# Kernel tuning notes

Measured on AMD Instinct MI355X. Metric: run time of the kernel, lower is better.

The kernel has to match this reference:

```python
import jax, jax.numpy as jnp
import numpy as np


def setup_inputs() -> dict:
    key = jax.random.key(0)
    k_h, k_w1, k_w2 = jax.random.split(key, 3)
    B, S, D = 8, 2048, 1024
    H = 2 * D  # reasoning_net hidden width
    # xavier_uniform-style scaled weights
    lim1 = float(np.sqrt(6.0 / (D + H)))
    lim2 = float(np.sqrt(6.0 / (H + D)))
    return {
        "hidden_states": jax.random.normal(k_h, (B, S, D), dtype=jnp.float32),
        "W1": jax.random.uniform(k_w1, (D, H), dtype=jnp.float32, minval=-lim1, maxval=lim1),
        "b1": jnp.zeros((H,), dtype=jnp.float32),
        "W2": jax.random.uniform(k_w2, (H, D), dtype=jnp.float32, minval=-lim2, maxval=lim2),
        "b2": jnp.zeros((D,), dtype=jnp.float32),
    }


def reference(hidden_states, W1, b1, W2, b2):
    """Chain reasoning forward.

    The torch loop carries output[:, -1:], but reasoning_net is a per-token MLP
    (Linear over the last dim), so processed[:, -1:] == MLP(current token) and the
    carried state never influences appended outputs. Faithful closed form:
      out[:, 0]  = hidden_states[:, 0]
      out[:, i]  = MLP(hidden_states[:, i])  for i >= 1
    Dropout is identity (eval). GELU is exact (torch default).
    """
    rest = hidden_states[:, 1:, :]  # [B, S-1, D]
    h = jax.nn.gelu(jnp.einsum("bsd,dh->bsh", rest, W1) + b1, approximate=False)
    out_rest = jnp.einsum("bsh,hd->bsd", h, W2) + b2
    return jnp.concatenate([hidden_states[:, :1, :], out_rest], axis=1)
```

## Files before the change

kernel.cpp:

```cpp
#include <hip/hip_runtime.h>
#include <hip/hip_bf16.h>
#include <cstdint>
#include <cstddef>

typedef unsigned short u16;
typedef __attribute__((ext_vector_type(8))) __bf16 bf16x8;
typedef __attribute__((ext_vector_type(8))) unsigned short u16x8;
typedef __attribute__((ext_vector_type(4))) float f32x4;

__device__ __forceinline__ void gload_lds16(const void* g, void* l) {
    __builtin_amdgcn_global_load_lds(
        (const __attribute__((address_space(1))) unsigned int*)g,
        (__attribute__((address_space(3))) unsigned int*)l,
        16, 0, 0);
}

__device__ __forceinline__ u16 f2bf(float f) {
    union { float f; unsigned int u; } v; v.f = f;
    unsigned int r = v.u + 0x7fffu + ((v.u >> 16) & 1u);
    return (u16)(r >> 16);
}

__device__ __forceinline__ float gelu_tanh(float x) {
    const float z = 0.7978845608028654f * x * (1.0f + 0.044715f * x * x);
    const float t = __builtin_amdgcn_exp2f(2.885390081777927f * z);
    const float th = 1.0f - 2.0f * __builtin_amdgcn_rcpf(t + 1.0f);
    return 0.5f * x * (1.0f + th);
}

template <int GELU, int OUT_BF16, int SKIP_S>
__global__ void gemm_bt(const u16* __restrict__ A,
                        const u16* __restrict__ Bt,
                        const float* __restrict__ bias,
                        void* __restrict__ Cv,
                        int M, int N, int K, int row0) {
    __shared__ __align__(16) char smem[32768];
    u16* As = (u16*)smem;
    u16* Bs = (u16*)(smem + 16384);
    float* Ct = (float*)smem;

    const int tid  = threadIdx.x;
    const int lane = tid & 63;
    const int wave = tid >> 6;
    const int wm   = (wave >> 1) * 64;
    const int wn   = (wave & 1) * 64;
    const int mrow = lane & 15;
    const int half = lane >> 4;

    const size_t ldb = (size_t)K * 2;
    const char* Ab = (const char*)(A + (size_t)blockIdx.x * 128 * K);
    const char* Bb = (const char*)(Bt + (size_t)blockIdx.y * 128 * K);

    size_t goff[4];
    int loff[4];
#pragma unroll
    for (int i = 0; i < 4; ++i) {
        const int L = tid + 256 * i, r = L >> 3, s = L & 7;
        goff[i] = (size_t)r * ldb + (size_t)((s ^ (r & 7)) << 4);
        loff[i] = L << 4;
    }

    int alds[2][4], blds[2][4];
#pragma unroll
    for (int j = 0; j < 2; ++j)
#pragma unroll
        for (int t = 0; t < 4; ++t) {
            const int g = j * 4 + half;
            const int ra = wm + t * 16 + mrow;
            alds[j][t] = ra * 128 + ((g ^ (ra & 7)) << 4);
            const int rb = wn + t * 16 + mrow;
            blds[j][t] = rb * 128 + ((g ^ (rb & 7)) << 4);
        }

    f32x4 acc[4][4];
#pragma unroll
    for (int i = 0; i < 4; ++i)
#pragma unroll
        for (int j = 0; j < 4; ++j) acc[i][j] = f32x4{0.f, 0.f, 0.f, 0.f};

    for (int k0 = 0; k0 < K; k0 += 64) {
        const size_t kb = (size_t)k0 * 2;
#pragma unroll
        for (int i = 0; i < 4; ++i)
            gload_lds16(Ab + goff[i] + kb, (char*)As + loff[i]);
#pragma unroll
        for (int i = 0; i < 4; ++i)
            gload_lds16(Bb + goff[i] + kb, (char*)Bs + loff[i]);
        __syncthreads();

#pragma unroll
        for (int j = 0; j < 2; ++j) {
            bf16x8 af[4], bfr[4];
#pragma unroll
            for (int t = 0; t < 4; ++t) {
                af[t]  = *(const bf16x8*)((const char*)As + alds[j][t]);
                bfr[t] = *(const bf16x8*)((const char*)Bs + blds[j][t]);
            }
#pragma unroll
            for (int mi = 0; mi < 4; ++mi)
#pragma unroll
                for (int ni = 0; ni < 4; ++ni)
                    acc[mi][ni] = __builtin_amdgcn_mfma_f32_16x16x32_bf16(
                        af[mi], bfr[ni], acc[mi][ni], 0, 0, 0);
        }
        __syncthreads();
    }

    const int lrow0 = wm + half * 4;
    const int lcol0 = wn + mrow;
    const int growbase = blockIdx.x * 128;
    const int gcolbase = blockIdx.y * 128;
    const int rr_rd = tid >> 3, cs_rd = (tid & 7) * 16;

#pragma unroll
    for (int c = 0; c < 4; ++c) {
        __syncthreads();
        if ((wm >> 6) == (c >> 1)) {
            const int mi0 = (c & 1) * 2;
#pragma unroll
            for (int dmi = 0; dmi < 2; ++dmi) {
                const int mi = mi0 + dmi;
#pragma unroll
                for (int ni = 0; ni < 4; ++ni) {
                    const int col = lcol0 + ni * 16;
                    const float bv = bias[gcolbase + col];
#pragma unroll
                    for (int r = 0; r < 4; ++r) {
                        const int rr = (mi * 16 + lrow0 + r) & 31;
                        float v = acc[mi][ni][r] + bv;
                        if (GELU) v = gelu_tanh(v);
                        Ct[rr * 132 + col] = v;
                    }
                }
            }
        }
        __syncthreads();
        const int grow = growbase + 32 * c + rr_rd;
        const bool skip = SKIP_S && (((row0 + grow) & 2047) == 0);
        if (!skip) {
            const float* ct = &Ct[rr_rd * 132 + cs_rd];
            const f32x4 v0 = *(const f32x4*)(ct);
            const f32x4 v1 = *(const f32x4*)(ct + 4);
            const f32x4 v2 = *(const f32x4*)(ct + 8);
            const f32x4 v3 = *(const f32x4*)(ct + 12);
            if (OUT_BF16) {
                u16x8 lo, hi;
#pragma unroll
                for (int j = 0; j < 4; ++j) {
                    lo[j] = f2bf(v0[j]); lo[j + 4] = f2bf(v1[j]);
                    hi[j] = f2bf(v2[j]); hi[j + 4] = f2bf(v3[j]);
                }
                u16* p = (u16*)Cv + (size_t)grow * N + gcolbase + cs_rd;
                *(u16x8*)(p)     = lo;
                *(u16x8*)(p + 8) = hi;
            } else {
                float* p = (float*)Cv + (size_t)grow * N + gcolbase + cs_rd;
                *(f32x4*)(p)      = v0;
                *(f32x4*)(p + 4)  = v1;
                *(f32x4*)(p + 8)  = v2;
                *(f32x4*)(p + 12) = v3;
            }
        }
    }
}

__device__ __forceinline__ void tcvt_block(const float* __restrict__ src,
                                           u16* __restrict__ dst, int R, int C,
                                           int bx, int by, int x, int y,
                                           u16 (*t)[33]) {
    for (int i = 0; i < 32; i += 8)
        t[y + i][x] = f2bf(src[(size_t)(by + y + i) * C + (bx + x)]);
    __syncthreads();
    for (int i = 0; i < 32; i += 8)
        dst[(size_t)(bx + y + i) * R + (by + x)] = t[x][y + i];
}

__global__ void prep(const float* __restrict__ X, const float* __restrict__ W1,
                     const float* __restrict__ W2, u16* __restrict__ Xb,
                     u16* __restrict__ W1T, u16* __restrict__ W2T,
                     float* __restrict__ out, long long nX) {
    __shared__ u16 t[32][33];
    const int b = blockIdx.x, tid = threadIdx.x;
    const int x = tid & 31, y = tid >> 5;
    if (b < 2048) {
        tcvt_block(W1, W1T, 1024, 2048, (b & 63) * 32, (b >> 6) * 32, x, y, t);
    } else if (b < 4096) {
        const int bi = b - 2048;
        tcvt_block(W2, W2T, 2048, 1024, (bi & 31) * 32, (bi >> 5) * 32, x, y, t);
    } else if (b < 4104) {
        const size_t base = (size_t)(b - 4096) * 2048 * 1024;
        *(float4*)(out + base + tid * 4) = *(const float4*)(X + base + tid * 4);
    } else {
        const long long stride = (long long)4096 * 256 * 4;
        for (long long i = ((long long)(b - 4104) * 256 + tid) * 4; i < nX;
             i += stride) {
            const float4 v = *(const float4*)(X + i);
            ushort4 o;
            o.x = f2bf(v.x); o.y = f2bf(v.y); o.z = f2bf(v.z); o.w = f2bf(v.w);
            *(ushort4*)(Xb + i) = o;
        }
    }
}

extern "C" void kernel_launch(void* const* d_in, const int* in_sizes, int n_in,
                              void* d_out, int out_size, void* d_ws, size_t ws_size,
                              hipStream_t stream) {
    const float* X  = (const float*)d_in[0];
    const float* W1 = (const float*)d_in[1];
    const float* b1 = (const float*)d_in[2];
    const float* W2 = (const float*)d_in[3];
    const float* b2 = (const float*)d_in[4];
    float* out = (float*)d_out;

    const int B = 8, S = 2048, D = 1024, H = 2048;
    const int M = B * S;

    u16* W1T = (u16*)d_ws;
    u16* W2T = W1T + (size_t)H * D;
    u16* Xb  = W2T + (size_t)D * H;
    u16* Hb  = Xb + (size_t)M * D;
    const size_t wfixed = (size_t)H * D * 2 * 2 + (size_t)M * D * 2;
    size_t avail_rows = (ws_size > wfixed) ? (ws_size - wfixed) / ((size_t)H * 2) : 0;
    int CM = (int)((avail_rows / 128) * 128);
    if (CM > M) CM = M;
    if (CM < 128) CM = 128;

    prep<<<dim3(8200), dim3(256), 0, stream>>>(
        X, W1, W2, Xb, W1T, W2T, out, (long long)M * D);

    for (int m0 = 0; m0 < M; m0 += CM) {
        const int rows = (M - m0 < CM) ? (M - m0) : CM;
        dim3 g1(rows / 128, H / 128);
        gemm_bt<1, 1, 0><<<g1, dim3(256), 0, stream>>>(
            Xb + (size_t)m0 * D, W1T, b1, Hb, rows, H, D, m0);
        dim3 g2(rows / 128, D / 128);
        gemm_bt<0, 0, 1><<<g2, dim3(256), 0, stream>>>(
            Hb, W2T, b2, out + (size_t)m0 * D, rows, D, H, m0);
    }
}
```

Baseline: 297.6 us.

## Replace 128x128 GEMM with double-buffered 256x256 tile, 8-wave pipelined kernel

Swaps the simple 128x128 tile GEMM, which synchronised every K step, for a 256x256 tile kernel with 512 threads. It double-buffers 128 KB of LDS, issues global-to-LDS loads for the next K slice while MFMAs run on the current one, and raises MFMA priority with s_setprio. The larger tile is meant to raise arithmetic intensity and hide memory latency. The epilogue uses a swizzled LDS staging layout. The costs are heavy LDS use that limits occupancy, fewer blocks per grid (the second GEMM gets only 256 blocks), and fragile hand-written waitcnt and barrier scheduling.

```diff
diff --git a/kernel.cpp b/kernel.cpp
--- a/kernel.cpp
+++ b/kernel.cpp
@@ -1,11 +1,11 @@
 #include <hip/hip_runtime.h>
-#include <hip/hip_bf16.h>
 #include <cstdint>
 #include <cstddef>
 
 typedef unsigned short u16;
 typedef __attribute__((ext_vector_type(8))) __bf16 bf16x8;
 typedef __attribute__((ext_vector_type(8))) unsigned short u16x8;
+typedef __attribute__((ext_vector_type(4))) unsigned short u16x4;
 typedef __attribute__((ext_vector_type(4))) float f32x4;
 
 __device__ __forceinline__ void gload_lds16(const void* g, void* l) {
@@ -28,137 +28,199 @@
     return 0.5f * x * (1.0f + th);
 }
 
+
+#define STAGE(mb, hrow, kb, lbase)                                   \
+    {                                                                \
+        const char* _s = (mb) + (size_t)(hrow)*ldb + (kb);           \
+        gload_lds16(_s + soff[0], smem + (lbase) + ldst[0]);         \
+        gload_lds16(_s + soff[1], smem + (lbase) + ldst[1]);         \
+    }
+#define LOADA(bufo, mh)                                              \
+    _Pragma("unroll") for (int ks = 0; ks < 2; ++ks) {               \
+        const char* _p = smem + (bufo) + A0 + g2[ks] + (mh)*8192;    \
+        _Pragma("unroll") for (int m = 0; m < 4; ++m)                \
+            af[m][ks] = *(const bf16x8*)(_p + m * 2048);             \
+    }
+#define LOADB(bufo, nh)                                              \
+    _Pragma("unroll") for (int ks = 0; ks < 2; ++ks) {               \
+        const char* _p = smem + (bufo) + 32768 + B0 + g2[ks] + (nh)*4096; \
+        _Pragma("unroll") for (int n = 0; n < 2; ++n)                \
+            bf[(nh)*2 + n][ks] = *(const bf16x8*)(_p + n * 2048);    \
+    }
+#define QMFMA(MS, NS)                                                \
+    __builtin_amdgcn_s_setprio(1);                                   \
+    _Pragma("unroll") for (int ks = 0; ks < 2; ++ks)                 \
+    _Pragma("unroll") for (int m = 0; m < 4; ++m)                    \
+    _Pragma("unroll") for (int n = 0; n < 2; ++n)                    \
+        acc[(MS) + m][(NS) + n] = __builtin_amdgcn_mfma_f32_16x16x32_bf16( \
+            af[m][ks], bf[(NS) + n][ks], acc[(MS) + m][(NS) + n], 0, 0, 0); \
+    __builtin_amdgcn_s_setprio(0);
+#define BAR __builtin_amdgcn_s_barrier()
+#define SB0 __builtin_amdgcn_sched_barrier(0)
+#define LGKM0                                                        \
+    {                                                                \
+        asm volatile("s_waitcnt lgkmcnt(0)" ::: "memory");           \
+        SB0;                                                         \
+    }
+
 template <int GELU, int OUT_BF16, int SKIP_S>
-__global__ void gemm_bt(const u16* __restrict__ A,
-                        const u16* __restrict__ Bt,
-                        const float* __restrict__ bias,
-                        void* __restrict__ Cv,
-                        int M, int N, int K, int row0) {
-    __shared__ __align__(16) char smem[32768];
-    u16* As = (u16*)smem;
-    u16* Bs = (u16*)(smem + 16384);
+__global__ __launch_bounds__(512, 2) void gemm256(
+    const u16* __restrict__ A, const u16* __restrict__ Bt,
+    const float* __restrict__ bias, void* __restrict__ Cv,
+    int N, int K, int row0) {
+    __shared__ __align__(16) char smem[131072];
+
+    const int tid = threadIdx.x, lane = tid & 63, wave = tid >> 6;
+    const int wr = wave >> 2, wc = wave & 3;
+    const int mrow = lane & 15, half = lane >> 4;
+
+    const size_t ldb = (size_t)K * 2;
+    const char* Ab = (const char*)A + (size_t)blockIdx.x * 256 * ldb;
+    const char* Bb = (const char*)Bt + (size_t)blockIdx.y * 256 * ldb;
+
+    size_t soff[2];
+    int ldst[2];
+#pragma unroll
+    for (int i = 0; i < 2; ++i) {
+        const int L = tid + 512 * i, r = L >> 3, s = L & 7;
+        soff[i] = (size_t)r * ldb + (size_t)((s ^ (r & 7)) << 4);
+        ldst[i] = L << 4;
+    }
+
+    const int A0 = (wr * 128 + mrow) * 128;
+    const int B0 = (wc * 64 + mrow) * 128;
+    int g2[2];
+#pragma unroll
+    for (int ks = 0; ks < 2; ++ks) g2[ks] = ((ks * 4 + half) ^ (mrow & 7)) << 4;
+
+    f32x4 acc[8][4];
+#pragma unroll
+    for (int i = 0; i < 8; ++i)
+#pragma unroll
+        for (int j = 0; j < 4; ++j) acc[i][j] = f32x4{0.f, 0.f, 0.f, 0.f};
+
+    bf16x8 af[4][2], bf[4][2];
+
+    STAGE(Ab, 0, 0, 0)
+    STAGE(Ab, 128, 0, 16384)
+    STAGE(Bb, 0, 0, 32768)
+    STAGE(Bb, 128, 0, 49152)
+    STAGE(Bb, 0, 128, 98304)
+    STAGE(Bb, 128, 0 + 128, 114688)
+    asm volatile("s_waitcnt vmcnt(4)" ::: "memory");
+    SB0;
+    BAR;
+    SB0;
+
+    const int niter = K >> 7;
+    for (int it = 0; it < niter; ++it) {
+        const bool last = (it == niter - 1);
+        const size_t kb1 = (size_t)(2 * it + 1) << 7;
+        const size_t kb2 = kb1 + 128, kb3 = kb1 + 256;
+        LOADA(0, 0)
+        LOADB(0, 0)
+        STAGE(Ab, 0, kb1, 65536)
+        BAR;
+        LGKM0
+        QMFMA(0, 0)
+        BAR;
+        LOADB(0, 1)
+        STAGE(Ab, 128, kb1, 81920)
+        BAR;
+        LGKM0
+        QMFMA(0, 2)
+        BAR;
+        LOADA(0, 1)
+        if (!last) STAGE(Bb, 0, kb2, 32768)
+        BAR;
+        LGKM0
+        QMFMA(4, 0)
+        BAR;
+        if (!last) STAGE(Bb, 128, kb2, 49152)
+        BAR;
+        QMFMA(4, 2)
+        if (last) {
+            asm volatile("s_waitcnt vmcnt(0)" ::: "memory");
+        } else {
+            asm volatile("s_waitcnt vmcnt(4)" ::: "memory");
+        }
+        SB0;
+        BAR;
+        SB0;
+        LOADA(65536, 0)
+        LOADB(65536, 0)
+        if (!last) STAGE(Ab, 0, kb2, 0)
+        BAR;
+        LGKM0
+        QMFMA(0, 0)
+        BAR;
+        LOADB(65536, 1)
+        if (!last) STAGE(Ab, 128, kb2, 16384)
+        BAR;
+        LGKM0
+        QMFMA(0, 2)
+        BAR;
+        LOADA(65536, 1)
+        if (!last) STAGE(Bb, 0, kb3, 98304)
+        BAR;
+        LGKM0
+        QMFMA(4, 0)
+        BAR;
+        if (!last) STAGE(Bb, 128, kb3, 114688)
+        BAR;
+        QMFMA(4, 2)
+        if (!last) asm volatile("s_waitcnt vmcnt(4)" ::: "memory");
+        SB0;
+        BAR;
+        SB0;
+    }
+
+    const int growbase = blockIdx.x * 256, gcolbase = blockIdx.y * 256;
     float* Ct = (float*)smem;
-
-    const int tid  = threadIdx.x;
-    const int lane = tid & 63;
-    const int wave = tid >> 6;
-    const int wm   = (wave >> 1) * 64;
-    const int wn   = (wave & 1) * 64;
-    const int mrow = lane & 15;
-    const int half = lane >> 4;
-
-    const size_t ldb = (size_t)K * 2;
-    const char* Ab = (const char*)(A + (size_t)blockIdx.x * 128 * K);
-    const char* Bb = (const char*)(Bt + (size_t)blockIdx.y * 128 * K);
-
-    size_t goff[4];
-    int loff[4];
-#pragma unroll
-    for (int i = 0; i < 4; ++i) {
-        const int L = tid + 256 * i, r = L >> 3, s = L & 7;
-        goff[i] = (size_t)r * ldb + (size_t)((s ^ (r & 7)) << 4);
-        loff[i] = L << 4;
-    }
-
-    int alds[2][4], blds[2][4];
-#pragma unroll
-    for (int j = 0; j < 2; ++j)
-#pragma unroll
-        for (int t = 0; t < 4; ++t) {
-            const int g = j * 4 + half;
-            const int ra = wm + t * 16 + mrow;
-            alds[j][t] = ra * 128 + ((g ^ (ra & 7)) << 4);
-            const int rb = wn + t * 16 + mrow;
-            blds[j][t] = rb * 128 + ((g ^ (rb & 7)) << 4);
-        }
-
-    f32x4 acc[4][4];
-#pragma unroll
-    for (int i = 0; i < 4; ++i)
-#pragma unroll
-        for (int j = 0; j < 4; ++j) acc[i][j] = f32x4{0.f, 0.f, 0.f, 0.f};
-
-    for (int k0 = 0; k0 < K; k0 += 64) {
-        const size_t kb = (size_t)k0 * 2;
-#pragma unroll
-        for (int i = 0; i < 4; ++i)
-            gload_lds16(Ab + goff[i] + kb, (char*)As + loff[i]);
-#pragma unroll
-        for (int i = 0; i < 4; ++i)
-            gload_lds16(Bb + goff[i] + kb, (char*)Bs + loff[i]);
-        __syncthreads();
-
-#pragma unroll
-        for (int j = 0; j < 2; ++j) {
-            bf16x8 af[4], bfr[4];
-#pragma unroll
-            for (int t = 0; t < 4; ++t) {
-                af[t]  = *(const bf16x8*)((const char*)As + alds[j][t]);
-                bfr[t] = *(const bf16x8*)((const char*)Bs + blds[j][t]);
-            }
-#pragma unroll
-            for (int mi = 0; mi < 4; ++mi)
-#pragma unroll
-                for (int ni = 0; ni < 4; ++ni)
-                    acc[mi][ni] = __builtin_amdgcn_mfma_f32_16x16x32_bf16(
-                        af[mi], bfr[ni], acc[mi][ni], 0, 0, 0);
-        }
-        __syncthreads();
-    }
-
-    const int lrow0 = wm + half * 4;
-    const int lcol0 = wn + mrow;
-    const int growbase = blockIdx.x * 128;
-    const int gcolbase = blockIdx.y * 128;
-    const int rr_rd = tid >> 3, cs_rd = (tid & 7) * 16;
-
+    const int rr = tid >> 3, gb = tid & 7, r7 = rr & 7;
 #pragma unroll
     for (int c = 0; c < 4; ++c) {
         __syncthreads();
-        if ((wm >> 6) == (c >> 1)) {
-            const int mi0 = (c & 1) * 2;
-#pragma unroll
-            for (int dmi = 0; dmi < 2; ++dmi) {
-                const int mi = mi0 + dmi;
+        if (wr == (c >> 1)) {
+#pragma unroll
+            for (int dm = 0; dm < 4; ++dm) {
+                const int mi = (c & 1) * 4 + dm;
 #pragma unroll
                 for (int ni = 0; ni < 4; ++ni) {
-                    const int col = lcol0 + ni * 16;
+                    const int col = wc * 64 + ni * 16 + mrow;
                     const float bv = bias[gcolbase + col];
 #pragma unroll
                     for (int r = 0; r < 4; ++r) {
-                        const int rr = (mi * 16 + lrow0 + r) & 31;
+                        const int rloc = dm * 16 + half * 4 + r;
                         float v = acc[mi][ni][r] + bv;
                         if (GELU) v = gelu_tanh(v);
-                        Ct[rr * 132 + col] = v;
+                        Ct[rloc * 256 +
+                           ((((col >> 2) ^ (rloc & 7)) << 2) | (col & 3))] = v;
                     }
                 }
             }
         }
         __syncthreads();
-        const int grow = growbase + 32 * c + rr_rd;
-        const bool skip = SKIP_S && (((row0 + grow) & 2047) == 0);
-        if (!skip) {
-            const float* ct = &Ct[rr_rd * 132 + cs_rd];
-            const f32x4 v0 = *(const f32x4*)(ct);
-            const f32x4 v1 = *(const f32x4*)(ct + 4);
-            const f32x4 v2 = *(const f32x4*)(ct + 8);
-            const f32x4 v3 = *(const f32x4*)(ct + 12);
+        const int grow = growbase + 64 * c + rr;
+        if (!(SKIP_S && (((row0 + grow) & 2047) == 0))) {
+            f32x4 v[8];
+#pragma unroll
+            for (int j = 0; j < 8; ++j)
+                v[j] = *(const f32x4*)(Ct + rr * 256 +
+                                       (((gb ^ r7) + 8 * j) << 2));
             if (OUT_BF16) {
-                u16x8 lo, hi;
-#pragma unroll
-                for (int j = 0; j < 4; ++j) {
-                    lo[j] = f2bf(v0[j]); lo[j + 4] = f2bf(v1[j]);
-                    hi[j] = f2bf(v2[j]); hi[j + 4] = f2bf(v3[j]);
+                u16* p = (u16*)Cv + (size_t)grow * N + gcolbase + gb * 4;
+#pragma unroll
+                for (int j = 0; j < 8; ++j) {
+                    u16x4 o;
+#pragma unroll
+                    for (int e = 0; e < 4; ++e) o[e] = f2bf(v[j][e]);
+                    *(u16x4*)(p + 32 * j) = o;
                 }
-                u16* p = (u16*)Cv + (size_t)grow * N + gcolbase + cs_rd;
-                *(u16x8*)(p)     = lo;
-                *(u16x8*)(p + 8) = hi;
             } else {
-                float* p = (float*)Cv + (size_t)grow * N + gcolbase + cs_rd;
-                *(f32x4*)(p)      = v0;
-                *(f32x4*)(p + 4)  = v1;
-                *(f32x4*)(p + 8)  = v2;
-                *(f32x4*)(p + 12) = v3;
+                float* p = (float*)Cv + (size_t)grow * N + gcolbase + gb * 4;
+#pragma unroll
+                for (int j = 0; j < 8; ++j) *(f32x4*)(p + 32 * j) = v[j];
             }
         }
     }
@@ -221,20 +283,20 @@
     u16* Hb  = Xb + (size_t)M * D;
     const size_t wfixed = (size_t)H * D * 2 * 2 + (size_t)M * D * 2;
     size_t avail_rows = (ws_size > wfixed) ? (ws_size - wfixed) / ((size_t)H * 2) : 0;
-    int CM = (int)((avail_rows / 128) * 128);
+    int CM = (int)((avail_rows / 256) * 256);
     if (CM > M) CM = M;
-    if (CM < 128) CM = 128;
+    if (CM < 256) CM = 256;
 
     prep<<<dim3(8200), dim3(256), 0, stream>>>(
         X, W1, W2, Xb, W1T, W2T, out, (long long)M * D);
 
     for (int m0 = 0; m0 < M; m0 += CM) {
         const int rows = (M - m0 < CM) ? (M - m0) : CM;
-        dim3 g1(rows / 128, H / 128);
-        gemm_bt<1, 1, 0><<<g1, dim3(256), 0, stream>>>(
-            Xb + (size_t)m0 * D, W1T, b1, Hb, rows, H, D, m0);
-        dim3 g2(rows / 128, D / 128);
-        gemm_bt<0, 0, 1><<<g2, dim3(256), 0, stream>>>(
-            Hb, W2T, b2, out + (size_t)m0 * D, rows, D, H, m0);
-    }
-}
+        dim3 g1(rows / 256, H / 256);
+        gemm256<1, 1, 0><<<g1, dim3(512), 0, stream>>>(
+            Xb + (size_t)m0 * D, W1T, b1, Hb, H, D, m0);
+        dim3 g2(rows / 256, D / 256);
+        gemm256<0, 0, 1><<<g2, dim3(512), 0, stream>>>(
+            Hb, W2T, b2, out + (size_t)m0 * D, D, H, m0);
+    }
+}
```

Measured after the change: 282.6 us. -5.0%, faster.
